# Performance work log

Measured on AMD Instinct MI355X. Metric: run time of the kernel, lower is better.

The kernel has to match this reference:

```python
import jax, jax.numpy as jnp
import numpy as np
from jax import lax

Q = 16384      # num questions (hyperedges)
S = 16384      # num students (nodes)
F = 64         # feat_dim
EMB = 64       # emb_dim
H = 32         # student_hist_max
C = 16384      # student_attn_chunk_size
E = 393216     # incidence edges per channel (24 chunks)


def setup_inputs() -> dict:
    key = jax.random.key(0)
    ks = jax.random.split(key, 24)
    rn = lambda k, sh, s=1.0: jax.random.normal(k, sh, dtype=jnp.float32) * s
    ri = lambda k, sh, hi: jax.random.randint(k, sh, 0, hi, dtype=jnp.int32)
    return {
        'x': rn(ks[0], (Q, F)),
        's_emb': rn(ks[1], (S, F)),
        'W_Q': rn(ks[2], (2 * F, F), 0.05), 'b_Q': jnp.zeros((F,), jnp.float32),
        'W_K': rn(ks[3], (F, F), 0.05),     'b_K': jnp.zeros((F,), jnp.float32),
        'W_V': rn(ks[4], (F, F), 0.05),     'b_V': jnp.zeros((F,), jnp.float32),
        'W_fuse': rn(ks[5], (2 * F, F), 0.05), 'b_fuse': jnp.zeros((F,), jnp.float32),
        'W_K2': rn(ks[6], (F, F), 0.05),    'b_K2': jnp.zeros((F,), jnp.float32),
        'W_V2': rn(ks[7], (F, F), 0.05),    'b_V2': jnp.zeros((F,), jnp.float32),
        'W_proj': rn(ks[8], (2 * F, EMB), 0.05), 'b_proj': jnp.zeros((EMB,), jnp.float32),
        'h1_bias': jnp.zeros((2, F), jnp.float32),  # nn.init.zeros_ in source
        'h2_bias': jnp.zeros((2, F), jnp.float32),
        'hist_qid_pos': ri(ks[9], (S, H), Q),
        'hist_cnt_pos': ri(ks[10], (S,), H + 1),
        'hist_qid_neg': ri(ks[11], (S, H), Q),
        'hist_cnt_neg': ri(ks[12], (S,), H + 1),
        'edge_sid_pos': ri(ks[13], (E,), S),
        'edge_qid_pos': ri(ks[14], (E,), Q),
        'edge_sid_neg': ri(ks[15], (E,), S),
        'edge_qid_neg': ri(ks[16], (E,), Q),
    }


def reference(x, s_emb, W_Q, b_Q, W_K, b_K, W_V, b_V, W_fuse, b_fuse,
              W_K2, b_K2, W_V2, b_V2, W_proj, b_proj, h1_bias, h2_bias,
              hist_qid_pos, hist_cnt_pos, hist_qid_neg, hist_cnt_neg,
              edge_sid_pos, edge_qid_pos, edge_sid_neg, edge_qid_neg):
    scale = jnp.float32(1.0 / np.sqrt(F))
    NEG = jnp.float32(-1e9)

    def channel(hist_qid, hist_cnt, e_sid, e_qid, ch):
        # dense per-student history keys/values: [S, H, F]
        xh = x[hist_qid]
        Kh = xh @ W_K + b_K + h1_bias[ch]
        Vh = xh @ W_V + b_V
        mask = jnp.arange(H, dtype=jnp.int32)[None, :] < hist_cnt[:, None]  # [S,H]

        def chunk_fn(args):
            sid, qid = args  # [C]
            # edge-level query: W_Q([x_q || e_u])
            q = jnp.concatenate([x[qid], s_emb[sid]], axis=-1) @ W_Q + b_Q  # [C,F]
            sc = jnp.einsum('cf,chf->ch', q, Kh[sid]) * scale               # [C,H]
            m = mask[sid]
            a = jax.nn.softmax(jnp.where(m, sc, NEG), axis=-1)
            a = jnp.where(m, a, 0.0)  # empty history -> zero output
            return jnp.einsum('ch,chf->cf', a, Vh[sid])                     # [C,F]

        nchunks = E // C
        agg = lax.map(chunk_fn, (e_sid.reshape(nchunks, C), e_qid.reshape(nchunks, C)))
        agg = agg.reshape(E, F)
        # fuse student embedding with history-aggregated context
        s_repr = jnp.concatenate([s_emb[e_sid], agg], axis=-1) @ W_fuse + b_fuse  # [E,F]
        # hop 2: question attends over its member students (segment softmax over e_qid)
        k2 = s_repr @ W_K2 + b_K2 + h2_bias[ch]
        v2 = s_repr @ W_V2 + b_V2
        sc2 = jnp.sum(x[e_qid] * k2, axis=-1) * scale                      # [E]
        mx = jax.ops.segment_max(sc2, e_qid, num_segments=Q)
        ex = jnp.exp(sc2 - mx[e_qid])
        den = jax.ops.segment_sum(ex, e_qid, num_segments=Q)
        alpha = ex / jnp.maximum(den[e_qid], 1e-9)
        return jax.ops.segment_sum(alpha[:, None] * v2, e_qid, num_segments=Q)  # [Q,F]

    pos = channel(hist_qid_pos, hist_cnt_pos, edge_sid_pos, edge_qid_pos, 0)
    neg = channel(hist_qid_neg, hist_cnt_neg, edge_sid_neg, edge_qid_neg, 1)
    return jnp.concatenate([pos, neg], axis=-1) @ W_proj + b_proj  # [Q, EMB]
```

## Files before the change

kernel.cpp:

```cpp
#include <hip/hip_runtime.h>

typedef float v2f __attribute__((ext_vector_type(2)));
typedef float v4f __attribute__((ext_vector_type(4)));

#define QN 16384
#define SN 16384
#define HN 32
#define EN 393216
#define KPAD 68

__global__ __launch_bounds__(256) void prep_kernel(
    const float* __restrict__ x, const float* __restrict__ s_emb,
    const float* __restrict__ W_Q, const float* __restrict__ b_Q,
    const float* __restrict__ W_K, const float* __restrict__ b_K,
    const float* __restrict__ W_V, const float* __restrict__ b_V,
    const float* __restrict__ W_fuse, const float* __restrict__ b_fuse,
    const float* __restrict__ W_K2, const float* __restrict__ b_K2,
    const float* __restrict__ h1b, const float* __restrict__ h2b,
    const int* __restrict__ es_pos, const int* __restrict__ es_neg,
    float* __restrict__ xKpos, float* __restrict__ xKneg,
    float* __restrict__ xVfp, float* __restrict__ xQ1, float* __restrict__ xq2p,
    float* __restrict__ c2pos, float* __restrict__ c2neg,
    float* __restrict__ sQ, float* __restrict__ sfp,
    int* __restrict__ cnt_pos, int* __restrict__ cnt_neg)
{
  __shared__ float xs[512];
  __shared__ float vs[512];
  __shared__ float wk2t[64 * 66];
  const int bid = blockIdx.x;
  const int t = threadIdx.x;
  const int j = t & 31, r = t >> 5;

  if (bid < 2048) {
    const int q = bid * 8 + r;
    if (t < 128) *(v4f*)&xs[t * 4] = *(const v4f*)&x[bid * 512 + t * 4];
    for (int i = 0; i < 16; i++) {
      int idx = i * 256 + t;
      wk2t[(idx & 63) * 66 + (idx >> 6)] = W_K2[idx];
    }
    __syncthreads();

    v2f accK = *(const v2f*)&b_K[2 * j];
    v2f accV = *(const v2f*)&b_V[2 * j];
    v2f accQ = {0.f, 0.f};
    float a2x = 0.f, a2y = 0.f;
    for (int g = 0; g < 64; g++) {
      float xv = xs[r * 64 + g];
      accK += xv * *(const v2f*)&W_K[g * 64 + 2 * j];
      accV += xv * *(const v2f*)&W_V[g * 64 + 2 * j];
      accQ += xv * *(const v2f*)&W_Q[g * 64 + 2 * j];
      a2x += xv * wk2t[g * 66 + j];
      a2y += xv * wk2t[g * 66 + j + 32];
    }
    *(v2f*)&xKpos[q * 64 + 2 * j] = accK + *(const v2f*)&h1b[2 * j];
    *(v2f*)&xKneg[q * 64 + 2 * j] = accK + *(const v2f*)&h1b[64 + 2 * j];
    *(v2f*)&xQ1[q * 64 + 2 * j] = accQ;
    v2f a2 = {a2x, a2y};
    *(v2f*)&xq2p[q * 64 + 2 * j] = a2;
    *(v2f*)&vs[r * 64 + 2 * j] = accV;

    v2f xv2 = *(const v2f*)&xs[r * 64 + 2 * j];
    v2f bb0 = *(const v2f*)&b_K2[2 * j] + *(const v2f*)&h2b[2 * j];
    v2f bb1 = *(const v2f*)&b_K2[2 * j] + *(const v2f*)&h2b[64 + 2 * j];
    v2f t0 = xv2 * bb0, t1 = xv2 * bb1;
    float p0 = t0.x + t0.y, p1v = t1.x + t1.y;
    for (int k = 16; k >= 1; k >>= 1) {
      p0 += __shfl_xor(p0, k, 32);
      p1v += __shfl_xor(p1v, k, 32);
    }
    if (j == 0) { c2pos[q] = p0 * 0.125f; c2neg[q] = p1v * 0.125f; }

    __syncthreads();
    float vfx = 0.f, vfy = 0.f;
    for (int g = 0; g < 64; g++) {
      float vv = vs[r * 64 + g];
      vfx += vv * W_fuse[(64 + g) * 64 + j];
      vfy += vv * W_fuse[(64 + g) * 64 + j + 32];
    }
    v2f vf = {vfx, vfy};
    *(v2f*)&xVfp[q * 64 + 2 * j] = vf;
  } else if (bid < 4096) {
    const int b2 = bid - 2048;
    const int s = b2 * 8 + r;
    if (t < 128) *(v4f*)&xs[t * 4] = *(const v4f*)&s_emb[b2 * 512 + t * 4];
    __syncthreads();
    v2f aq = *(const v2f*)&b_Q[2 * j];
    float afx = b_fuse[j], afy = b_fuse[j + 32];
    for (int g = 0; g < 64; g++) {
      float v = xs[r * 64 + g];
      aq += v * *(const v2f*)&W_Q[(64 + g) * 64 + 2 * j];
      afx += v * W_fuse[g * 64 + j];
      afy += v * W_fuse[g * 64 + j + 32];
    }
    *(v2f*)&sQ[s * 64 + 2 * j] = aq;
    v2f af = {afx, afy};
    *(v2f*)&sfp[s * 64 + 2 * j] = af;
  } else {
    const int hb = bid - 4096;
    const bool neg = hb >= 1536;
    const int* __restrict__ sid = neg ? es_neg : es_pos;
    int* __restrict__ cnt = neg ? cnt_neg : cnt_pos;
    const int i = (neg ? hb - 1536 : hb) * 256 + t;
    atomicAdd(&cnt[sid[i]], 1);
  }
}

__global__ __launch_bounds__(256) void scan_kernel(
    const int* __restrict__ cnt_pos, int* __restrict__ beg_pos, int* __restrict__ cur_pos,
    const int* __restrict__ cnt_neg, int* __restrict__ beg_neg, int* __restrict__ cur_neg) {
  const int* cnt = blockIdx.y ? cnt_neg : cnt_pos;
  int* beg = blockIdx.y ? beg_neg : beg_pos;
  int* cur = blockIdx.y ? cur_neg : cur_pos;
  __shared__ int part[256];
  int t = threadIdx.x;
  int s = 0;
  for (int i = 0; i < 64; i++) s += cnt[i * 256 + t];
  part[t] = s;
  __syncthreads();
  for (int off = 1; off < 256; off <<= 1) {
    int v = (t >= off) ? part[t - off] : 0;
    __syncthreads();
    part[t] += v;
    __syncthreads();
  }
  int run = part[t] - s;
  for (int i = 0; i < 64; i++) {
    int id = i * 256 + t;
    int c = cnt[id];
    beg[id] = run; cur[id] = run;
    run += c;
  }
}

__global__ __launch_bounds__(256) void scatter_kernel(
    const int* __restrict__ sid_pos, const int* __restrict__ qid_pos,
    int* __restrict__ cur_pos, int* __restrict__ csr_pos,
    const int* __restrict__ sid_neg, const int* __restrict__ qid_neg,
    int* __restrict__ cur_neg, int* __restrict__ csr_neg, int n) {
  const int* sid = blockIdx.y ? sid_neg : sid_pos;
  const int* qid = blockIdx.y ? qid_neg : qid_pos;
  int* cursor = blockIdx.y ? cur_neg : cur_pos;
  int* csr_qid = blockIdx.y ? csr_neg : csr_pos;
  int i = blockIdx.x * 256 + threadIdx.x;
  if (i < n) {
    int p = atomicAdd(&cursor[sid[i]], 1);
    csr_qid[p] = qid[i];
  }
}

__global__ __launch_bounds__(256, 4) void main_kernel(
    const float* __restrict__ xKpos, const float* __restrict__ xKneg,
    const float* __restrict__ xVfp, const float* __restrict__ xQ1,
    const float* __restrict__ xq2p,
    const float* __restrict__ c2pos, const float* __restrict__ c2neg,
    const float* __restrict__ sQ, const float* __restrict__ sfp,
    const int* __restrict__ hq_pos, const int* __restrict__ hc_pos,
    const int* __restrict__ hq_neg, const int* __restrict__ hc_neg,
    const int* __restrict__ beg_pos, const int* __restrict__ cntS_pos,
    const int* __restrict__ csr_pos,
    const int* __restrict__ beg_neg, const int* __restrict__ cntS_neg,
    const int* __restrict__ csr_neg,
    float* __restrict__ num_pos, float* __restrict__ den_pos,
    float* __restrict__ num_neg, float* __restrict__ den_neg)
{
  const int s = blockIdx.x;
  const int ch = blockIdx.y;
  const float* __restrict__ xK = ch ? xKneg : xKpos;
  const float* __restrict__ c2 = ch ? c2neg : c2pos;
  const int* __restrict__ hq = ch ? hq_neg : hq_pos;
  const int* __restrict__ hc = ch ? hc_neg : hc_pos;
  const int* __restrict__ beg = ch ? beg_neg : beg_pos;
  const int* __restrict__ cntS = ch ? cntS_neg : cntS_pos;
  const int* __restrict__ csr = ch ? csr_neg : csr_pos;
  float* __restrict__ num = ch ? num_neg : num_pos;
  float* __restrict__ den = ch ? den_neg : den_pos;

  const int t = threadIdx.x;
  __shared__ float Kl[HN * KPAD];
  __shared__ float Vl[HN * 64];
  __shared__ float Qg[8 * 4 * 64];
  __shared__ float Al[8 * 32 * 4];
  __shared__ float sQl[64], sflp[64];
  __shared__ int hql[HN];

  const int hcnt = hc[s];
  if (t < HN) hql[t] = hq[s * HN + t];
  if (t >= 128 && t < 192) sQl[t - 128] = sQ[s * 64 + (t - 128)];
  if (t >= 192) sflp[t - 192] = sfp[s * 64 + (t - 192)];
  __syncthreads();
  for (int i = 0; i < 2; i++) {
    int idx = i * 256 + t;
    int h = idx >> 4, jj = idx & 15;
    int row = hql[h];
    *(v4f*)&Kl[h * KPAD + jj * 4] = *(const v4f*)&xK[row * 64 + jj * 4];
    *(v4f*)&Vl[h * 64 + jj * 4] = *(const v4f*)&xVfp[row * 64 + jj * 4];
  }
  const int ebeg = beg[s];
  const int ne = cntS[s];
  __syncthreads();

  const float scale = 0.125f;
  const int g = t >> 5;
  const int c = t & 31;
  float* __restrict__ Qb = &Qg[g * 256];
  float* __restrict__ Ab = &Al[g * 128];
  const v4f* kp = (const v4f*)&Kl[c * KPAD];
  const v2f sqv = *(const v2f*)&sQl[2 * c];
  const v2f sfv = *(const v2f*)&sflp[2 * c];

  for (int i0 = g * 4; i0 < ne; i0 += 32) {
    const int nb = ne - i0;
    int q0 = 0, q1 = 0, q2 = 0, q3 = 0;
    q0 = csr[ebeg + i0];
    { v2f qv = *(const v2f*)&xQ1[q0 * 64 + 2 * c] + sqv; *(v2f*)&Qb[2 * c] = qv; }
    if (nb > 1) { q1 = csr[ebeg + i0 + 1]; v2f qv = *(const v2f*)&xQ1[q1 * 64 + 2 * c] + sqv; *(v2f*)&Qb[64 + 2 * c] = qv; }
    if (nb > 2) { q2 = csr[ebeg + i0 + 2]; v2f qv = *(const v2f*)&xQ1[q2 * 64 + 2 * c] + sqv; *(v2f*)&Qb[128 + 2 * c] = qv; }
    if (nb > 3) { q3 = csr[ebeg + i0 + 3]; v2f qv = *(const v2f*)&xQ1[q3 * 64 + 2 * c] + sqv; *(v2f*)&Qb[192 + 2 * c] = qv; }

    float s0 = 0.f, s1 = 0.f, s2 = 0.f, s3 = 0.f;
#pragma unroll 4
    for (int k = 0; k < 16; k++) {
      v4f k4 = kp[k];
      v4f qa = ((const v4f*)&Qb[0])[k];
      s0 += qa.x * k4.x + qa.y * k4.y + qa.z * k4.z + qa.w * k4.w;
      v4f qb = ((const v4f*)&Qb[64])[k];
      s1 += qb.x * k4.x + qb.y * k4.y + qb.z * k4.z + qb.w * k4.w;
      v4f qc = ((const v4f*)&Qb[128])[k];
      s2 += qc.x * k4.x + qc.y * k4.y + qc.z * k4.z + qc.w * k4.w;
      v4f qd = ((const v4f*)&Qb[192])[k];
      s3 += qd.x * k4.x + qd.y * k4.y + qd.z * k4.z + qd.w * k4.w;
    }
    const bool valid = (c < hcnt);
    float e0 = valid ? __expf(s0 * scale) : 0.f;
    float e1 = valid ? __expf(s1 * scale) : 0.f;
    float e2 = valid ? __expf(s2 * scale) : 0.f;
    float e3 = valid ? __expf(s3 * scale) : 0.f;
    float d0 = e0, d1 = e1, d2 = e2, d3 = e3;
    for (int k = 16; k >= 1; k >>= 1) {
      d0 += __shfl_xor(d0, k, 32);
      d1 += __shfl_xor(d1, k, 32);
      d2 += __shfl_xor(d2, k, 32);
      d3 += __shfl_xor(d3, k, 32);
    }
    v4f av;
    av.x = (d0 > 0.f) ? e0 / d0 : 0.f;
    av.y = (d1 > 0.f) ? e1 / d1 : 0.f;
    av.z = (d2 > 0.f) ? e2 / d2 : 0.f;
    av.w = (d3 > 0.f) ? e3 / d3 : 0.f;
    *(v4f*)&Ab[c * 4] = av;

    v2f r0 = sfv, r1 = sfv, r2 = sfv, r3 = sfv;
#pragma unroll 8
    for (int h = 0; h < HN; h++) {
      v2f vv = *(const v2f*)&Vl[h * 64 + 2 * c];
      v4f a4 = *(const v4f*)&Ab[h * 4];
      r0 += a4.x * vv;
      r1 += a4.y * vv;
      r2 += a4.z * vv;
      r3 += a4.w * vv;
    }

    {
      v2f x2 = *(const v2f*)&xq2p[q0 * 64 + 2 * c];
      float p = r0.x * x2.x + r0.y * x2.y;
      for (int k = 16; k >= 1; k >>= 1) p += __shfl_xor(p, k, 32);
      float ew = __expf(p * scale + c2[q0]);
      atomicAdd(&num[q0 * 64 + c], ew * r0.x);
      atomicAdd(&num[q0 * 64 + 32 + c], ew * r0.y);
      if (c == 0) atomicAdd(&den[q0], ew);
    }
    if (nb > 1) {
      v2f x2 = *(const v2f*)&xq2p[q1 * 64 + 2 * c];
      float p = r1.x * x2.x + r1.y * x2.y;
      for (int k = 16; k >= 1; k >>= 1) p += __shfl_xor(p, k, 32);
      float ew = __expf(p * scale + c2[q1]);
      atomicAdd(&num[q1 * 64 + c], ew * r1.x);
      atomicAdd(&num[q1 * 64 + 32 + c], ew * r1.y);
      if (c == 0) atomicAdd(&den[q1], ew);
    }
    if (nb > 2) {
      v2f x2 = *(const v2f*)&xq2p[q2 * 64 + 2 * c];
      float p = r2.x * x2.x + r2.y * x2.y;
      for (int k = 16; k >= 1; k >>= 1) p += __shfl_xor(p, k, 32);
      float ew = __expf(p * scale + c2[q2]);
      atomicAdd(&num[q2 * 64 + c], ew * r2.x);
      atomicAdd(&num[q2 * 64 + 32 + c], ew * r2.y);
      if (c == 0) atomicAdd(&den[q2], ew);
    }
    if (nb > 3) {
      v2f x2 = *(const v2f*)&xq2p[q3 * 64 + 2 * c];
      float p = r3.x * x2.x + r3.y * x2.y;
      for (int k = 16; k >= 1; k >>= 1) p += __shfl_xor(p, k, 32);
      float ew = __expf(p * scale + c2[q3]);
      atomicAdd(&num[q3 * 64 + c], ew * r3.x);
      atomicAdd(&num[q3 * 64 + 32 + c], ew * r3.y);
      if (c == 0) atomicAdd(&den[q3], ew);
    }
  }
}

__global__ __launch_bounds__(256) void final_kernel(
    const float* __restrict__ num_pos, const float* __restrict__ den_pos,
    const float* __restrict__ num_neg, const float* __restrict__ den_neg,
    const float* __restrict__ W_V2, const float* __restrict__ b_V2,
    const float* __restrict__ W_proj, const float* __restrict__ b_proj,
    float* __restrict__ out)
{
  __shared__ float np[8 * 64], nn[8 * 64], hp[8 * 64], hn[8 * 64];
  int t = threadIdx.x;
  int j = t & 31, r = t >> 5;
  int q = blockIdx.x * 8 + r;
  if (t < 128) {
    *(v4f*)&np[t * 4] = *(const v4f*)&num_pos[blockIdx.x * 512 + t * 4];
    *(v4f*)&nn[t * 4] = *(const v4f*)&num_neg[blockIdx.x * 512 + t * 4];
  }
  __syncthreads();
  float dp = den_pos[q], dn = den_neg[q];
  float ip = (dp > 0.f) ? 1.f / dp : 0.f;
  float in_ = (dn > 0.f) ? 1.f / dn : 0.f;
  v2f zero = {0.f, 0.f};
  v2f bv = *(const v2f*)&b_V2[2 * j];
  v2f hpv = (dp > 0.f) ? bv : zero;
  v2f hnv = (dn > 0.f) ? bv : zero;
  for (int f = 0; f < 64; f++) {
    v2f w = *(const v2f*)&W_V2[f * 64 + 2 * j];
    hpv += (np[r * 64 + f] * ip) * w;
    hnv += (nn[r * 64 + f] * in_) * w;
  }
  *(v2f*)&hp[r * 64 + 2 * j] = hpv;
  *(v2f*)&hn[r * 64 + 2 * j] = hnv;
  __syncthreads();
  v2f o = *(const v2f*)&b_proj[2 * j];
  for (int f = 0; f < 64; f++) {
    o += hp[r * 64 + f] * *(const v2f*)&W_proj[f * 64 + 2 * j];
    o += hn[r * 64 + f] * *(const v2f*)&W_proj[(64 + f) * 64 + 2 * j];
  }
  *(v2f*)&out[q * 64 + 2 * j] = o;
}

extern "C" void kernel_launch(void* const* d_in, const int* in_sizes, int n_in,
                              void* d_out, int out_size, void* d_ws, size_t ws_size,
                              hipStream_t stream) {
  const float* x      = (const float*)d_in[0];
  const float* s_emb  = (const float*)d_in[1];
  const float* W_Q    = (const float*)d_in[2];
  const float* b_Q    = (const float*)d_in[3];
  const float* W_K    = (const float*)d_in[4];
  const float* b_K    = (const float*)d_in[5];
  const float* W_V    = (const float*)d_in[6];
  const float* b_V    = (const float*)d_in[7];
  const float* W_fuse = (const float*)d_in[8];
  const float* b_fuse = (const float*)d_in[9];
  const float* W_K2   = (const float*)d_in[10];
  const float* b_K2   = (const float*)d_in[11];
  const float* W_V2   = (const float*)d_in[12];
  const float* b_V2   = (const float*)d_in[13];
  const float* W_proj = (const float*)d_in[14];
  const float* b_proj = (const float*)d_in[15];
  const float* h1b    = (const float*)d_in[16];
  const float* h2b    = (const float*)d_in[17];
  const int* hq_pos   = (const int*)d_in[18];
  const int* hc_pos   = (const int*)d_in[19];
  const int* hq_neg   = (const int*)d_in[20];
  const int* hc_neg   = (const int*)d_in[21];
  const int* es_pos   = (const int*)d_in[22];
  const int* eq_pos   = (const int*)d_in[23];
  const int* es_neg   = (const int*)d_in[24];
  const int* eq_neg   = (const int*)d_in[25];
  float* out = (float*)d_out;

  size_t off = 0;
  char* base = (char*)d_ws;
  auto carve = [&](size_t bytes) -> void* {
    void* p = base + off;
    off += (bytes + 255) & ~(size_t)255;
    return p;
  };
  float* num_pos = (float*)carve((size_t)QN * 64 * 4);
  float* num_neg = (float*)carve((size_t)QN * 64 * 4);
  float* den_pos = (float*)carve((size_t)QN * 4);
  float* den_neg = (float*)carve((size_t)QN * 4);
  int* cnt_pos   = (int*)carve((size_t)SN * 4);
  int* cnt_neg   = (int*)carve((size_t)SN * 4);
  size_t zero_bytes = off;
  float* xKpos = (float*)carve((size_t)QN * 64 * 4);
  float* xKneg = (float*)carve((size_t)QN * 64 * 4);
  float* xVfp  = (float*)carve((size_t)QN * 64 * 4);
  float* xQ1   = (float*)carve((size_t)QN * 64 * 4);
  float* xq2p  = (float*)carve((size_t)QN * 64 * 4);
  float* sQ    = (float*)carve((size_t)SN * 64 * 4);
  float* sfp   = (float*)carve((size_t)SN * 64 * 4);
  float* c2pos = (float*)carve((size_t)QN * 4);
  float* c2neg = (float*)carve((size_t)QN * 4);
  int* beg_pos = (int*)carve((size_t)SN * 4);
  int* beg_neg = (int*)carve((size_t)SN * 4);
  int* cur_pos = (int*)carve((size_t)SN * 4);
  int* cur_neg = (int*)carve((size_t)SN * 4);
  int* csr_pos = (int*)carve((size_t)EN * 4);
  int* csr_neg = (int*)carve((size_t)EN * 4);
  if (off > ws_size) return;

  hipMemsetAsync(d_ws, 0, zero_bytes, stream);

  prep_kernel<<<4096 + 2 * (EN / 256), 256, 0, stream>>>(
      x, s_emb, W_Q, b_Q, W_K, b_K, W_V, b_V, W_fuse, b_fuse, W_K2, b_K2,
      h1b, h2b, es_pos, es_neg,
      xKpos, xKneg, xVfp, xQ1, xq2p, c2pos, c2neg, sQ, sfp,
      cnt_pos, cnt_neg);

  scan_kernel<<<dim3(1, 2), 256, 0, stream>>>(cnt_pos, beg_pos, cur_pos,
                                              cnt_neg, beg_neg, cur_neg);
  scatter_kernel<<<dim3(EN / 256, 2), 256, 0, stream>>>(es_pos, eq_pos, cur_pos, csr_pos,
                                                        es_neg, eq_neg, cur_neg, csr_neg, EN);

  main_kernel<<<dim3(SN, 2), 256, 0, stream>>>(
      xKpos, xKneg, xVfp, xQ1, xq2p, c2pos, c2neg, sQ, sfp,
      hq_pos, hc_pos, hq_neg, hc_neg,
      beg_pos, cnt_pos, csr_pos, beg_neg, cnt_neg, csr_neg,
      num_pos, den_pos, num_neg, den_neg);

  final_kernel<<<QN / 8, 256, 0, stream>>>(num_pos, den_pos, num_neg, den_neg,
                                           W_V2, b_V2, W_proj, b_proj, out);
}
```

Before: 607.8 us.

## Software-pipeline edge gathers in main kernel and raise occupancy hint

```diff
diff --git a/kernel.cpp b/kernel.cpp
--- a/kernel.cpp
+++ b/kernel.cpp
@@ -148,7 +148,24 @@
   }
 }
 
-__global__ __launch_bounds__(256, 4) void main_kernel(
+#define LDBATCH(BASE, Q0,Q1,Q2,Q3, A0,A1,A2,A3, X0,X1,X2,X3, C0,C1,C2,C3) do { \
+    int _m = ne - 1; \
+    Q0 = csr[ebeg + (BASE)]; \
+    Q1 = csr[ebeg + min((BASE) + 1, _m)]; \
+    Q2 = csr[ebeg + min((BASE) + 2, _m)]; \
+    Q3 = csr[ebeg + min((BASE) + 3, _m)]; \
+    A0 = *(const v2f*)&xQ1[(size_t)Q0 * 64 + 2 * c] + sqv; \
+    A1 = *(const v2f*)&xQ1[(size_t)Q1 * 64 + 2 * c] + sqv; \
+    A2 = *(const v2f*)&xQ1[(size_t)Q2 * 64 + 2 * c] + sqv; \
+    A3 = *(const v2f*)&xQ1[(size_t)Q3 * 64 + 2 * c] + sqv; \
+    X0 = *(const v2f*)&xq2p[(size_t)Q0 * 64 + 2 * c]; \
+    X1 = *(const v2f*)&xq2p[(size_t)Q1 * 64 + 2 * c]; \
+    X2 = *(const v2f*)&xq2p[(size_t)Q2 * 64 + 2 * c]; \
+    X3 = *(const v2f*)&xq2p[(size_t)Q3 * 64 + 2 * c]; \
+    C0 = c2[Q0]; C1 = c2[Q1]; C2 = c2[Q2]; C3 = c2[Q3]; \
+  } while (0)
+
+__global__ __launch_bounds__(256, 5) void main_kernel(
     const float* __restrict__ xKpos, const float* __restrict__ xKneg,
     const float* __restrict__ xVfp, const float* __restrict__ xQ1,
     const float* __restrict__ xq2p,
@@ -180,20 +197,17 @@
   __shared__ float Vl[HN * 64];
   __shared__ float Qg[8 * 4 * 64];
   __shared__ float Al[8 * 32 * 4];
-  __shared__ float sQl[64], sflp[64];
   __shared__ int hql[HN];
 
   const int hcnt = hc[s];
   if (t < HN) hql[t] = hq[s * HN + t];
-  if (t >= 128 && t < 192) sQl[t - 128] = sQ[s * 64 + (t - 128)];
-  if (t >= 192) sflp[t - 192] = sfp[s * 64 + (t - 192)];
   __syncthreads();
   for (int i = 0; i < 2; i++) {
     int idx = i * 256 + t;
     int h = idx >> 4, jj = idx & 15;
     int row = hql[h];
-    *(v4f*)&Kl[h * KPAD + jj * 4] = *(const v4f*)&xK[row * 64 + jj * 4];
-    *(v4f*)&Vl[h * 64 + jj * 4] = *(const v4f*)&xVfp[row * 64 + jj * 4];
+    *(v4f*)&Kl[h * KPAD + jj * 4] = *(const v4f*)&xK[(size_t)row * 64 + jj * 4];
+    *(v4f*)&Vl[h * 64 + jj * 4] = *(const v4f*)&xVfp[(size_t)row * 64 + jj * 4];
   }
   const int ebeg = beg[s];
   const int ne = cntS[s];
@@ -205,96 +219,112 @@
   float* __restrict__ Qb = &Qg[g * 256];
   float* __restrict__ Ab = &Al[g * 128];
   const v4f* kp = (const v4f*)&Kl[c * KPAD];
-  const v2f sqv = *(const v2f*)&sQl[2 * c];
-  const v2f sfv = *(const v2f*)&sflp[2 * c];
-
-  for (int i0 = g * 4; i0 < ne; i0 += 32) {
-    const int nb = ne - i0;
-    int q0 = 0, q1 = 0, q2 = 0, q3 = 0;
-    q0 = csr[ebeg + i0];
-    { v2f qv = *(const v2f*)&xQ1[q0 * 64 + 2 * c] + sqv; *(v2f*)&Qb[2 * c] = qv; }
-    if (nb > 1) { q1 = csr[ebeg + i0 + 1]; v2f qv = *(const v2f*)&xQ1[q1 * 64 + 2 * c] + sqv; *(v2f*)&Qb[64 + 2 * c] = qv; }
-    if (nb > 2) { q2 = csr[ebeg + i0 + 2]; v2f qv = *(const v2f*)&xQ1[q2 * 64 + 2 * c] + sqv; *(v2f*)&Qb[128 + 2 * c] = qv; }
-    if (nb > 3) { q3 = csr[ebeg + i0 + 3]; v2f qv = *(const v2f*)&xQ1[q3 * 64 + 2 * c] + sqv; *(v2f*)&Qb[192 + 2 * c] = qv; }
-
-    float s0 = 0.f, s1 = 0.f, s2 = 0.f, s3 = 0.f;
+  const v2f sqv = *(const v2f*)&sQ[(size_t)s * 64 + 2 * c];
+  const v2f sfv = *(const v2f*)&sfp[(size_t)s * 64 + 2 * c];
+
+  int i0 = g * 4;
+  if (i0 < ne) {
+    int q0, q1, q2, q3;
+    v2f a0, a1, a2, a3, x20, x21, x22, x23;
+    float cc0, cc1, cc2, cc3;
+    LDBATCH(i0, q0, q1, q2, q3, a0, a1, a2, a3, x20, x21, x22, x23, cc0, cc1, cc2, cc3);
+
+    for (; i0 < ne; i0 += 32) {
+      const int nb = ne - i0;
+      *(v2f*)&Qb[2 * c] = a0;
+      *(v2f*)&Qb[64 + 2 * c] = a1;
+      *(v2f*)&Qb[128 + 2 * c] = a2;
+      *(v2f*)&Qb[192 + 2 * c] = a3;
+
+      int n0, n1, n2, n3;
+      v2f na0, na1, na2, na3, nx0, nx1, nx2, nx3;
+      float nc0, nc1, nc2, nc3;
+      const bool more = (i0 + 32) < ne;
+      if (more) {
+        LDBATCH(i0 + 32, n0, n1, n2, n3, na0, na1, na2, na3,
+                nx0, nx1, nx2, nx3, nc0, nc1, nc2, nc3);
+      }
+
+      float s0 = 0.f, s1 = 0.f, s2 = 0.f, s3 = 0.f;
 #pragma unroll 4
-    for (int k = 0; k < 16; k++) {
-      v4f k4 = kp[k];
-      v4f qa = ((const v4f*)&Qb[0])[k];
-      s0 += qa.x * k4.x + qa.y * k4.y + qa.z * k4.z + qa.w * k4.w;
-      v4f qb = ((const v4f*)&Qb[64])[k];
-      s1 += qb.x * k4.x + qb.y * k4.y + qb.z * k4.z + qb.w * k4.w;
-      v4f qc = ((const v4f*)&Qb[128])[k];
-      s2 += qc.x * k4.x + qc.y * k4.y + qc.z * k4.z + qc.w * k4.w;
-      v4f qd = ((const v4f*)&Qb[192])[k];
-      s3 += qd.x * k4.x + qd.y * k4.y + qd.z * k4.z + qd.w * k4.w;
-    }
-    const bool valid = (c < hcnt);
-    float e0 = valid ? __expf(s0 * scale) : 0.f;
-    float e1 = valid ? __expf(s1 * scale) : 0.f;
-    float e2 = valid ? __expf(s2 * scale) : 0.f;
-    float e3 = valid ? __expf(s3 * scale) : 0.f;
-    float d0 = e0, d1 = e1, d2 = e2, d3 = e3;
-    for (int k = 16; k >= 1; k >>= 1) {
-      d0 += __shfl_xor(d0, k, 32);
-      d1 += __shfl_xor(d1, k, 32);
-      d2 += __shfl_xor(d2, k, 32);
-      d3 += __shfl_xor(d3, k, 32);
-    }
-    v4f av;
-    av.x = (d0 > 0.f) ? e0 / d0 : 0.f;
-    av.y = (d1 > 0.f) ? e1 / d1 : 0.f;
-    av.z = (d2 > 0.f) ? e2 / d2 : 0.f;
-    av.w = (d3 > 0.f) ? e3 / d3 : 0.f;
-    *(v4f*)&Ab[c * 4] = av;
-
-    v2f r0 = sfv, r1 = sfv, r2 = sfv, r3 = sfv;
+      for (int k = 0; k < 16; k++) {
+        v4f k4 = kp[k];
+        v4f qa = ((const v4f*)&Qb[0])[k];
+        s0 += qa.x * k4.x + qa.y * k4.y + qa.z * k4.z + qa.w * k4.w;
+        v4f qb = ((const v4f*)&Qb[64])[k];
+        s1 += qb.x * k4.x + qb.y * k4.y + qb.z * k4.z + qb.w * k4.w;
+        v4f qc = ((const v4f*)&Qb[128])[k];
+        s2 += qc.x * k4.x + qc.y * k4.y + qc.z * k4.z + qc.w * k4.w;
+        v4f qd = ((const v4f*)&Qb[192])[k];
+        s3 += qd.x * k4.x + qd.y * k4.y + qd.z * k4.z + qd.w * k4.w;
+      }
+      const bool valid = (c < hcnt);
+      float e0 = valid ? __expf(s0 * scale) : 0.f;
+      float e1 = valid ? __expf(s1 * scale) : 0.f;
+      float e2 = valid ? __expf(s2 * scale) : 0.f;
+      float e3 = valid ? __expf(s3 * scale) : 0.f;
+      float d0 = e0, d1 = e1, d2 = e2, d3 = e3;
+      for (int k = 16; k >= 1; k >>= 1) {
+        d0 += __shfl_xor(d0, k, 32);
+        d1 += __shfl_xor(d1, k, 32);
+        d2 += __shfl_xor(d2, k, 32);
+        d3 += __shfl_xor(d3, k, 32);
+      }
+      v4f av;
+      av.x = (d0 > 0.f) ? e0 / d0 : 0.f;
+      av.y = (d1 > 0.f) ? e1 / d1 : 0.f;
+      av.z = (d2 > 0.f) ? e2 / d2 : 0.f;
+      av.w = (d3 > 0.f) ? e3 / d3 : 0.f;
+      *(v4f*)&Ab[c * 4] = av;
+
+      v2f r0 = sfv, r1 = sfv, r2 = sfv, r3 = sfv;
 #pragma unroll 8
-    for (int h = 0; h < HN; h++) {
-      v2f vv = *(const v2f*)&Vl[h * 64 + 2 * c];
-      v4f a4 = *(const v4f*)&Ab[h * 4];
-      r0 += a4.x * vv;
-      r1 += a4.y * vv;
-      r2 += a4.z * vv;
-      r3 += a4.w * vv;
-    }
-
-    {
-      v2f x2 = *(const v2f*)&xq2p[q0 * 64 + 2 * c];
-      float p = r0.x * x2.x + r0.y * x2.y;
-      for (int k = 16; k >= 1; k >>= 1) p += __shfl_xor(p, k, 32);
-      float ew = __expf(p * scale + c2[q0]);
-      atomicAdd(&num[q0 * 64 + c], ew * r0.x);
-      atomicAdd(&num[q0 * 64 + 32 + c], ew * r0.y);
-      if (c == 0) atomicAdd(&den[q0], ew);
-    }
-    if (nb > 1) {
-      v2f x2 = *(const v2f*)&xq2p[q1 * 64 + 2 * c];
-      float p = r1.x * x2.x + r1.y * x2.y;
-      for (int k = 16; k >= 1; k >>= 1) p += __shfl_xor(p, k, 32);
-      float ew = __expf(p * scale + c2[q1]);
-      atomicAdd(&num[q1 * 64 + c], ew * r1.x);
-      atomicAdd(&num[q1 * 64 + 32 + c], ew * r1.y);
-      if (c == 0) atomicAdd(&den[q1], ew);
-    }
-    if (nb > 2) {
-      v2f x2 = *(const v2f*)&xq2p[q2 * 64 + 2 * c];
-      float p = r2.x * x2.x + r2.y * x2.y;
-      for (int k = 16; k >= 1; k >>= 1) p += __shfl_xor(p, k, 32);
-      float ew = __expf(p * scale + c2[q2]);
-      atomicAdd(&num[q2 * 64 + c], ew * r2.x);
-      atomicAdd(&num[q2 * 64 + 32 + c], ew * r2.y);
-      if (c == 0) atomicAdd(&den[q2], ew);
-    }
-    if (nb > 3) {
-      v2f x2 = *(const v2f*)&xq2p[q3 * 64 + 2 * c];
-      float p = r3.x * x2.x + r3.y * x2.y;
-      for (int k = 16; k >= 1; k >>= 1) p += __shfl_xor(p, k, 32);
-      float ew = __expf(p * scale + c2[q3]);
-      atomicAdd(&num[q3 * 64 + c], ew * r3.x);
-      atomicAdd(&num[q3 * 64 + 32 + c], ew * r3.y);
-      if (c == 0) atomicAdd(&den[q3], ew);
+      for (int h = 0; h < HN; h++) {
+        v2f vv = *(const v2f*)&Vl[h * 64 + 2 * c];
+        v4f a4 = *(const v4f*)&Ab[h * 4];
+        r0 += a4.x * vv;
+        r1 += a4.y * vv;
+        r2 += a4.z * vv;
+        r3 += a4.w * vv;
+      }
+
+      {
+        float p = r0.x * x20.x + r0.y * x20.y;
+        for (int k = 16; k >= 1; k >>= 1) p += __shfl_xor(p, k, 32);
+        float ew = __expf(p * scale + cc0);
+        atomicAdd(&num[(size_t)q0 * 64 + c], ew * r0.x);
+        atomicAdd(&num[(size_t)q0 * 64 + 32 + c], ew * r0.y);
+        if (c == 0) atomicAdd(&den[q0], ew);
+      }
+      if (nb > 1) {
+        float p = r1.x * x21.x + r1.y * x21.y;
+        for (int k = 16; k >= 1; k >>= 1) p += __shfl_xor(p, k, 32);
+        float ew = __expf(p * scale + cc1);
+        atomicAdd(&num[(size_t)q1 * 64 + c], ew * r1.x);
+        atomicAdd(&num[(size_t)q1 * 64 + 32 + c], ew * r1.y);
+        if (c == 0) atomicAdd(&den[q1], ew);
+      }
+      if (nb > 2) {
+        float p = r2.x * x22.x + r2.y * x22.y;
+        for (int k = 16; k >= 1; k >>= 1) p += __shfl_xor(p, k, 32);
+        float ew = __expf(p * scale + cc2);
+        atomicAdd(&num[(size_t)q2 * 64 + c], ew * r2.x);
+        atomicAdd(&num[(size_t)q2 * 64 + 32 + c], ew * r2.y);
+        if (c == 0) atomicAdd(&den[q2], ew);
+      }
+      if (nb > 3) {
+        float p = r3.x * x23.x + r3.y * x23.y;
+        for (int k = 16; k >= 1; k >>= 1) p += __shfl_xor(p, k, 32);
+        float ew = __expf(p * scale + cc3);
+        atomicAdd(&num[(size_t)q3 * 64 + c], ew * r3.x);
+        atomicAdd(&num[(size_t)q3 * 64 + 32 + c], ew * r3.y);
+        if (c == 0) atomicAdd(&den[q3], ew);
+      }
+
+      q0 = n0; q1 = n1; q2 = n2; q3 = n3;
+      a0 = na0; a1 = na1; a2 = na2; a3 = na3;
+      x20 = nx0; x21 = nx1; x22 = nx2; x23 = nx3;
+      cc0 = nc0; cc1 = nc1; cc2 = nc2; cc3 = nc3;
     }
   }
 }
```

New measurement: 602.4 us. No clear change (-0.9%).
